# Kernel optimization log

Hardware: AMD Instinct MI355X
Metric: run time of the kernel (lower is better)

The kernel has to match this reference:

```python
import jax, jax.numpy as jnp
from jax import lax
import numpy as np

N_ASSETS = 256
BATCH = 512
MAX_WEIGHT = 0.05
N_ITERS = 300       # FISTA iterations (fixed, jit-friendly)
BISECT_ITERS = 60   # bisection iterations for the simplex-box projection
POWER_ITERS = 30    # power iterations for Lipschitz constant


def _project_capped_simplex(v, c):
    """Project rows of v onto {w : sum(w)=1, -c <= w <= c}.

    Finds tau s.t. sum(clip(v - tau, -c, c)) = 1 by bisection (non-diff),
    then recomputes tau exactly from the active-set mask so the projection
    is correctly differentiable (piecewise-linear Jacobian).
    """
    vs = lax.stop_gradient(v)
    lo = jnp.min(vs, axis=-1) - c   # sum = +n*c > 1 here
    hi = jnp.max(vs, axis=-1) + c   # sum = -n*c < 1 here

    def bis(carry, _):
        lo, hi = carry
        mid = 0.5 * (lo + hi)
        s = jnp.sum(jnp.clip(vs - mid[:, None], -c, c), axis=-1)
        lo = jnp.where(s > 1.0, mid, lo)
        hi = jnp.where(s > 1.0, hi, mid)
        return (lo, hi), None

    (lo, hi), _ = lax.scan(bis, (lo, hi), None, length=BISECT_ITERS)
    tau0 = 0.5 * (lo + hi)
    z = vs - tau0[:, None]
    interior = (jnp.abs(z) < c).astype(v.dtype)          # unclipped coords
    k_hi = jnp.sum((z >= c).astype(v.dtype), axis=-1)    # clipped at +c
    k_lo = jnp.sum((z <= -c).astype(v.dtype), axis=-1)   # clipped at -c
    denom = jnp.maximum(jnp.sum(interior, axis=-1), 1.0)
    # exact tau given the (stop-gradient) active set -> correct Jacobian in v
    tau = (jnp.sum(interior * v, axis=-1) + c * (k_hi - k_lo) - 1.0) / denom
    return jnp.clip(v - tau[:, None], -c, c)


def _min_var_weights(covmat_sqrt, c):
    """argmin_w ||A w||^2  s.t. sum(w)=1, -c<=w<=c  (batched FISTA)."""
    B, n, _ = covmat_sqrt.shape
    # Q = A^T A (the objective only depends on A through Q)
    Q = jnp.einsum('bij,bik->bjk', covmat_sqrt, covmat_sqrt)

    # power iteration for lambda_max(Q) -> step size 1/L, L = 2*lambda_max
    u = jnp.ones((B, n), covmat_sqrt.dtype) / jnp.sqrt(jnp.asarray(n, covmat_sqrt.dtype))

    def pit(u, _):
        u = jnp.einsum('bij,bj->bi', Q, u)
        u = u / (jnp.linalg.norm(u, axis=-1, keepdims=True) + 1e-12)
        return u, None

    u, _ = lax.scan(pit, u, None, length=POWER_ITERS)
    lmax = jnp.einsum('bi,bij,bj->b', u, Q, u)
    step = lax.stop_gradient(1.0 / (2.0 * lmax + 1e-12))[:, None]

    w0 = _project_capped_simplex(jnp.full((B, n), 1.0 / n, covmat_sqrt.dtype), c)

    @jax.checkpoint
    def fista(carry, _):
        w, y, t = carry
        g = 2.0 * jnp.einsum('bij,bj->bi', Q, y)
        w_new = _project_capped_simplex(y - step * g, c)
        t_new = 0.5 * (1.0 + jnp.sqrt(1.0 + 4.0 * t * t))
        y_new = w_new + ((t - 1.0) / t_new) * (w_new - w)
        return (w_new, y_new, t_new), None

    t0 = jnp.asarray(1.0, covmat_sqrt.dtype)
    (w, _, _), _ = lax.scan(fista, (w0, w0, t0), None, length=N_ITERS)
    return w


def setup_inputs() -> dict:
    key = jax.random.key(0)
    covmat_sqrt = jax.random.normal(
        key, (BATCH, N_ASSETS, N_ASSETS), dtype=jnp.float32
    ) / np.sqrt(N_ASSETS).astype(np.float32)
    return {"covmat_sqrt": covmat_sqrt}


def reference(covmat_sqrt):
    return _min_var_weights(covmat_sqrt, MAX_WEIGHT)
```

## Files before the change

kernel.cpp:

```cpp
#include <hip/hip_runtime.h>
#include <math.h>


#define NA    256
#define CAPW  0.05f

typedef float v2f __attribute__((ext_vector_type(2)));

template<int CTRL, int RM>
__device__ __forceinline__ float dpp0(float x) {
    return __int_as_float(__builtin_amdgcn_update_dpp(
        0, __float_as_int(x), CTRL, RM, 0xf, true));
}
template<int CTRL, int RM>
__device__ __forceinline__ float dppI(float x, float ident) {
    return __int_as_float(__builtin_amdgcn_update_dpp(
        __float_as_int(ident), __float_as_int(x), CTRL, RM, 0xf, false));
}
__device__ __forceinline__ float bcast63(float x) {
    return __int_as_float(__builtin_amdgcn_readlane(__float_as_int(x), 63));
}
__device__ __forceinline__ float wsum(float x) {
    x += dpp0<0x111, 0xf>(x);
    x += dpp0<0x112, 0xf>(x);
    x += dpp0<0x114, 0xf>(x);
    x += dpp0<0x118, 0xf>(x);
    x += dpp0<0x142, 0xa>(x);
    x += dpp0<0x143, 0xc>(x);
    return bcast63(x);
}
__device__ __forceinline__ float wmin(float x) {
    const float I = 1e30f;
    x = fminf(x, dppI<0x111, 0xf>(x, I));
    x = fminf(x, dppI<0x112, 0xf>(x, I));
    x = fminf(x, dppI<0x114, 0xf>(x, I));
    x = fminf(x, dppI<0x118, 0xf>(x, I));
    x = fminf(x, dppI<0x142, 0xa>(x, I));
    x = fminf(x, dppI<0x143, 0xc>(x, I));
    return bcast63(x);
}
__device__ __forceinline__ float wmax(float x) {
    const float I = -1e30f;
    x = fmaxf(x, dppI<0x111, 0xf>(x, I));
    x = fmaxf(x, dppI<0x112, 0xf>(x, I));
    x = fmaxf(x, dppI<0x114, 0xf>(x, I));
    x = fmaxf(x, dppI<0x118, 0xf>(x, I));
    x = fmaxf(x, dppI<0x142, 0xa>(x, I));
    x = fmaxf(x, dppI<0x143, 0xc>(x, I));
    return bcast63(x);
}

__global__ void __launch_bounds__(512, 2)
markowitz_fista(const float* __restrict__ A, float* __restrict__ out)
{
    __shared__ float A_lds[32 * 256];
    __shared__ float y_lds[256];
    __shared__ float p_lds[8 * 256];
    __shared__ int   done_flag;

    const int tid = threadIdx.x;
    const int b   = blockIdx.x;
    const int r4  = tid & 63;
    const int e   = tid >> 6;
    const int R0  = r4 * 4;
    const int C0  = e * 32;

    const float* __restrict__ Ab = A + (size_t)b * NA * NA;

    v2f q2[4][16];
    #pragma unroll
    for (int a = 0; a < 4; ++a)
        #pragma unroll
        for (int k = 0; k < 16; ++k) q2[a][k] = (v2f){0.0f, 0.0f};

    for (int it = 0; it < 8; ++it) {
        __syncthreads();
        const float4* src = (const float4*)(Ab + it * 32 * 256);
        float4* dst = (float4*)A_lds;
        #pragma unroll
        for (int qd = 0; qd < 4; ++qd) dst[qd * 512 + tid] = src[qd * 512 + tid];
        __syncthreads();
        for (int ii = 0; ii < 32; ++ii) {
            const float* row = A_lds + ii * 256;
            float4 rv = *(const float4*)(row + R0);
            v2f r0 = {rv.x, rv.x}, r1 = {rv.y, rv.y}, r2 = {rv.z, rv.z}, r3 = {rv.w, rv.w};
            #pragma unroll
            for (int cc = 0; cc < 8; ++cc) {
                float4 cv = *(const float4*)(row + C0 + 4 * cc);
                v2f clo = {cv.x, cv.y}, chi = {cv.z, cv.w};
                q2[0][2*cc  ] = __builtin_elementwise_fma(r0, clo, q2[0][2*cc  ]);
                q2[0][2*cc+1] = __builtin_elementwise_fma(r0, chi, q2[0][2*cc+1]);
                q2[1][2*cc  ] = __builtin_elementwise_fma(r1, clo, q2[1][2*cc  ]);
                q2[1][2*cc+1] = __builtin_elementwise_fma(r1, chi, q2[1][2*cc+1]);
                q2[2][2*cc  ] = __builtin_elementwise_fma(r2, clo, q2[2][2*cc  ]);
                q2[2][2*cc+1] = __builtin_elementwise_fma(r2, chi, q2[2][2*cc+1]);
                q2[3][2*cc  ] = __builtin_elementwise_fma(r3, clo, q2[3][2*cc  ]);
                q2[3][2*cc+1] = __builtin_elementwise_fma(r3, chi, q2[3][2*cc+1]);
            }
        }
    }

    auto partials = [&](bool chk) -> bool {
        __syncthreads();
        int fl = chk ? done_flag : 0;
        v2f aL0 = {0,0}, aL1 = {0,0}, aL2 = {0,0}, aL3 = {0,0};
        v2f aH0 = {0,0}, aH1 = {0,0}, aH2 = {0,0}, aH3 = {0,0};
        const float* yv = y_lds + C0;
        #pragma unroll
        for (int cc = 0; cc < 8; ++cc) {
            float4 y4 = *(const float4*)(yv + 4 * cc);
            v2f ylo = {y4.x, y4.y}, yhi = {y4.z, y4.w};
            aL0 = __builtin_elementwise_fma(q2[0][2*cc  ], ylo, aL0);
            aH0 = __builtin_elementwise_fma(q2[0][2*cc+1], yhi, aH0);
            aL1 = __builtin_elementwise_fma(q2[1][2*cc  ], ylo, aL1);
            aH1 = __builtin_elementwise_fma(q2[1][2*cc+1], yhi, aH1);
            aL2 = __builtin_elementwise_fma(q2[2][2*cc  ], ylo, aL2);
            aH2 = __builtin_elementwise_fma(q2[2][2*cc+1], yhi, aH2);
            aL3 = __builtin_elementwise_fma(q2[3][2*cc  ], ylo, aL3);
            aH3 = __builtin_elementwise_fma(q2[3][2*cc+1], yhi, aH3);
        }
        if (fl) return true;
        v2f s0 = aL0 + aH0, s1 = aL1 + aH1, s2 = aL2 + aH2, s3 = aL3 + aH3;
        *(float4*)(p_lds + e * 256 + R0) =
            make_float4(s0.x + s0.y, s1.x + s1.y, s2.x + s2.y, s3.x + s3.y);
        __syncthreads();
        return false;
    };
    auto reduceg = [&]() -> float4 {
        float4 r = *(const float4*)(p_lds + 4 * tid);
        #pragma unroll
        for (int ee = 1; ee < 8; ++ee) {
            float4 pv = *(const float4*)(p_lds + ee * 256 + 4 * tid);
            r.x += pv.x; r.y += pv.y; r.z += pv.z; r.w += pv.w;
        }
        return r;
    };

    if (tid < 64) {
        *(float4*)(y_lds + 4 * tid) = make_float4(0.0625f, 0.0625f, 0.0625f, 0.0625f);
    }
    float u0 = 0.f, u1 = 0.f, u2 = 0.f, u3 = 0.f;
    for (int p = 0; p < 30; ++p) {
        partials(false);
        if (tid < 64) {
            float4 g4 = reduceg();
            float ss = wsum(g4.x*g4.x + g4.y*g4.y + g4.z*g4.z + g4.w*g4.w);
            float inv = 1.0f / (sqrtf(ss) + 1e-12f);
            u0 = g4.x * inv; u1 = g4.y * inv; u2 = g4.z * inv; u3 = g4.w * inv;
            *(float4*)(y_lds + 4 * tid) = make_float4(u0, u1, u2, u3);
        }
    }
    partials(false);

    float step2 = 0.f, t = 1.0f, tau_ws = 0.0f, rm = 0.0f;
    float wa = 0.f, wb = 0.f, wc = 0.f, wd = 0.f;
    float ya = 0.f, yb = 0.f, yc = 0.f, yd = 0.f;
    if (tid < 64) {
        float4 g4 = reduceg();
        float lm = wsum(u0*g4.x + u1*g4.y + u2*g4.z + u3*g4.w);
        float step = 1.0f / (2.0f * lm + 1e-12f);
        step2 = 2.0f * step;
        wa = wb = wc = wd = 1.0f / 256.0f;
        ya = yb = yc = yd = 1.0f / 256.0f;
        *(float4*)(y_lds + 4 * tid) = make_float4(ya, yb, yc, yd);
    }
    if (tid == 0) done_flag = 0;

    for (int itn = 0; itn < 300; ++itn) {
        if (partials(true)) break;
        if (tid < 64) {
            float4 g4 = reduceg();
            float v0 = ya - step2 * g4.x;
            float v1 = yb - step2 * g4.y;
            float v2 = yc - step2 * g4.z;
            float v3 = yd - step2 * g4.w;

            float lo = wmin(fminf(fminf(v0, v1), fminf(v2, v3))) - CAPW;
            float hi = wmax(fmaxf(fmaxf(v0, v1), fmaxf(v2, v3))) + CAPW;
            float tau = fminf(fmaxf(tau_ws, lo), hi);

            float s = 0.f, cnt = 1.f, sm1 = 0.f;
            bool have = false;
            for (int ni = 0; ni < 10; ++ni) {
                float z0 = v0 - tau, z1 = v1 - tau, z2 = v2 - tau, z3 = v3 - tau;
                float c0 = fminf(fmaxf(z0, -CAPW), CAPW);
                float c1 = fminf(fmaxf(z1, -CAPW), CAPW);
                float c2 = fminf(fmaxf(z2, -CAPW), CAPW);
                float c3 = fminf(fmaxf(z3, -CAPW), CAPW);
                s   = wsum(c0 + c1 + c2 + c3);
                cnt = wsum((fabsf(z0) < CAPW ? 1.f : 0.f) +
                           (fabsf(z1) < CAPW ? 1.f : 0.f) +
                           (fabsf(z2) < CAPW ? 1.f : 0.f) +
                           (fabsf(z3) < CAPW ? 1.f : 0.f));
                sm1 = s - 1.0f;
                if (fabsf(sm1) <= 1e-5f) { have = true; break; }
                if (sm1 > 0.0f) lo = tau; else hi = tau;
                float tn2 = tau + sm1 / fmaxf(cnt, 1.0f);
                if (!(tn2 > lo && tn2 < hi)) tn2 = 0.5f * (lo + hi);
                tau = tn2;
            }
            if (!have) {
                float z0 = v0 - tau, z1 = v1 - tau, z2 = v2 - tau, z3 = v3 - tau;
                float c0 = fminf(fmaxf(z0, -CAPW), CAPW);
                float c1 = fminf(fmaxf(z1, -CAPW), CAPW);
                float c2 = fminf(fmaxf(z2, -CAPW), CAPW);
                float c3 = fminf(fmaxf(z3, -CAPW), CAPW);
                s   = wsum(c0 + c1 + c2 + c3);
                cnt = wsum((fabsf(z0) < CAPW ? 1.f : 0.f) +
                           (fabsf(z1) < CAPW ? 1.f : 0.f) +
                           (fabsf(z2) < CAPW ? 1.f : 0.f) +
                           (fabsf(z3) < CAPW ? 1.f : 0.f));
                sm1 = s - 1.0f;
            }
            float tauf = tau + sm1 / fmaxf(cnt, 1.0f);
            tau_ws = tauf;
            float w0n = fminf(fmaxf(v0 - tauf, -CAPW), CAPW);
            float w1n = fminf(fmaxf(v1 - tauf, -CAPW), CAPW);
            float w2n = fminf(fmaxf(v2 - tauf, -CAPW), CAPW);
            float w3n = fminf(fmaxf(v3 - tauf, -CAPW), CAPW);

            float tn = 0.5f * (1.0f + sqrtf(1.0f + 4.0f * t * t));
            float beta = (t - 1.0f) / tn;
            float y0n = w0n + beta * (w0n - wa);
            float y1n = w1n + beta * (w1n - wb);
            float y2n = w2n + beta * (w2n - wc);
            float y3n = w3n + beta * (w3n - wd);

            float dm = fmaxf(fmaxf(fabsf(w0n - wa), fabsf(w1n - wb)),
                             fmaxf(fabsf(w2n - wc), fabsf(w3n - wd)));
            rm = fmaxf(rm, dm);
            if ((itn & 7) == 7) {
                float rmax = wmax(rm);
                if (rmax < 1e-10f && tid == 0) done_flag = 1;
                rm = 0.0f;
            }

            wa = w0n; wb = w1n; wc = w2n; wd = w3n;
            ya = y0n; yb = y1n; yc = y2n; yd = y3n;
            t = tn;
            *(float4*)(y_lds + 4 * tid) = make_float4(ya, yb, yc, yd);
        }
    }

    if (tid < 64) {
        *(float4*)(out + b * 256 + 4 * tid) = make_float4(wa, wb, wc, wd);
    }
}

extern "C" void kernel_launch(void* const* d_in, const int* in_sizes, int n_in,
                              void* d_out, int out_size, void* d_ws, size_t ws_size,
                              hipStream_t stream) {
    (void)in_sizes; (void)n_in; (void)d_ws; (void)ws_size; (void)out_size;
    const float* A = (const float*)d_in[0];
    float* out = (float*)d_out;
    hipLaunchKernelGGL(markowitz_fista, dim3(512), dim3(512), 0, stream, A, out);
}
```

Measured before the change: 1.058 ms.

## Run projection redundantly in all waves and double-buffer partials to cut barriers

Every wave now redundantly performs the gradient reduction and capped-simplex projection, rather than only wave 0. Each wave publishes only the y slice that it itself consumes, so no cross-wave y handoff is needed. Partial sums are double-buffered, which lets each iteration use a single barrier instead of two, and the done flag becomes a per-wave early break. This removes idle waves waiting on wave 0 and one barrier per iteration, at the cost of duplicated scalar work and more LDS reads in the reduction.

```diff
diff --git a/kernel.cpp b/kernel.cpp
--- a/kernel.cpp
+++ b/kernel.cpp
@@ -54,16 +54,15 @@
 markowitz_fista(const float* __restrict__ A, float* __restrict__ out)
 {
     __shared__ float A_lds[32 * 256];
-    __shared__ float y_lds[256];
-    __shared__ float p_lds[8 * 256];
-    __shared__ int   done_flag;
-
-    const int tid = threadIdx.x;
-    const int b   = blockIdx.x;
-    const int r4  = tid & 63;
-    const int e   = tid >> 6;
-    const int R0  = r4 * 4;
-    const int C0  = e * 32;
+    __shared__ float p_lds[2][8 * 256];
+    __shared__ float y_sl[8 * 32];
+
+    const int tid  = threadIdx.x;
+    const int b    = blockIdx.x;
+    const int lane = tid & 63;
+    const int e    = tid >> 6;
+    const int R0   = lane * 4;
+    const int C0   = e * 32;
 
     const float* __restrict__ Ab = A + (size_t)b * NA * NA;
 
@@ -100,12 +99,15 @@
         }
     }
 
-    auto partials = [&](bool chk) -> bool {
-        __syncthreads();
-        int fl = chk ? done_flag : 0;
+    auto publish_y = [&](float y0v, float y1v, float y2v, float y3v) {
+        if ((lane >> 3) == e)
+            *(float4*)(y_sl + C0 + ((lane & 7) << 2)) = make_float4(y0v, y1v, y2v, y3v);
+    };
+
+    auto partials = [&](int buf) {
         v2f aL0 = {0,0}, aL1 = {0,0}, aL2 = {0,0}, aL3 = {0,0};
         v2f aH0 = {0,0}, aH1 = {0,0}, aH2 = {0,0}, aH3 = {0,0};
-        const float* yv = y_lds + C0;
+        const float* yv = y_sl + C0;
         #pragma unroll
         for (int cc = 0; cc < 8; ++cc) {
             float4 y4 = *(const float4*)(yv + 4 * cc);
@@ -119,131 +121,123 @@
             aL3 = __builtin_elementwise_fma(q2[3][2*cc  ], ylo, aL3);
             aH3 = __builtin_elementwise_fma(q2[3][2*cc+1], yhi, aH3);
         }
-        if (fl) return true;
         v2f s0 = aL0 + aH0, s1 = aL1 + aH1, s2 = aL2 + aH2, s3 = aL3 + aH3;
-        *(float4*)(p_lds + e * 256 + R0) =
+        *(float4*)(&p_lds[buf][e * 256 + R0]) =
             make_float4(s0.x + s0.y, s1.x + s1.y, s2.x + s2.y, s3.x + s3.y);
         __syncthreads();
-        return false;
     };
-    auto reduceg = [&]() -> float4 {
-        float4 r = *(const float4*)(p_lds + 4 * tid);
+    auto reduceg = [&](int buf) -> float4 {
+        float4 r = *(const float4*)(&p_lds[buf][R0]);
         #pragma unroll
         for (int ee = 1; ee < 8; ++ee) {
-            float4 pv = *(const float4*)(p_lds + ee * 256 + 4 * tid);
+            float4 pv = *(const float4*)(&p_lds[buf][ee * 256 + R0]);
             r.x += pv.x; r.y += pv.y; r.z += pv.z; r.w += pv.w;
         }
         return r;
     };
 
-    if (tid < 64) {
-        *(float4*)(y_lds + 4 * tid) = make_float4(0.0625f, 0.0625f, 0.0625f, 0.0625f);
-    }
-    float u0 = 0.f, u1 = 0.f, u2 = 0.f, u3 = 0.f;
+    float u0 = 0.0625f, u1 = 0.0625f, u2 = 0.0625f, u3 = 0.0625f;
+    publish_y(u0, u1, u2, u3);
+    int pb = 0;
     for (int p = 0; p < 30; ++p) {
-        partials(false);
-        if (tid < 64) {
-            float4 g4 = reduceg();
-            float ss = wsum(g4.x*g4.x + g4.y*g4.y + g4.z*g4.z + g4.w*g4.w);
-            float inv = 1.0f / (sqrtf(ss) + 1e-12f);
-            u0 = g4.x * inv; u1 = g4.y * inv; u2 = g4.z * inv; u3 = g4.w * inv;
-            *(float4*)(y_lds + 4 * tid) = make_float4(u0, u1, u2, u3);
-        }
-    }
-    partials(false);
-
-    float step2 = 0.f, t = 1.0f, tau_ws = 0.0f, rm = 0.0f;
-    float wa = 0.f, wb = 0.f, wc = 0.f, wd = 0.f;
-    float ya = 0.f, yb = 0.f, yc = 0.f, yd = 0.f;
-    if (tid < 64) {
-        float4 g4 = reduceg();
+        partials(pb);
+        float4 g4 = reduceg(pb); pb ^= 1;
+        float ss = wsum(g4.x*g4.x + g4.y*g4.y + g4.z*g4.z + g4.w*g4.w);
+        float inv = 1.0f / (sqrtf(ss) + 1e-12f);
+        u0 = g4.x * inv; u1 = g4.y * inv; u2 = g4.z * inv; u3 = g4.w * inv;
+        publish_y(u0, u1, u2, u3);
+    }
+    partials(pb);
+    {
+        float4 g4 = reduceg(pb); pb ^= 1;
         float lm = wsum(u0*g4.x + u1*g4.y + u2*g4.z + u3*g4.w);
         float step = 1.0f / (2.0f * lm + 1e-12f);
-        step2 = 2.0f * step;
-        wa = wb = wc = wd = 1.0f / 256.0f;
-        ya = yb = yc = yd = 1.0f / 256.0f;
-        *(float4*)(y_lds + 4 * tid) = make_float4(ya, yb, yc, yd);
-    }
-    if (tid == 0) done_flag = 0;
+        u0 = 2.0f * step;
+    }
+    const float step2 = u0;
+
+    float t = 1.0f, tau_ws = 0.0f, rm = 0.0f;
+    float wa = 1.0f/256.0f, wb = wa, wc = wa, wd = wa;
+    float ya = wa, yb = wa, yc = wa, yd = wa;
+    publish_y(ya, yb, yc, yd);
 
     for (int itn = 0; itn < 300; ++itn) {
-        if (partials(true)) break;
-        if (tid < 64) {
-            float4 g4 = reduceg();
-            float v0 = ya - step2 * g4.x;
-            float v1 = yb - step2 * g4.y;
-            float v2 = yc - step2 * g4.z;
-            float v3 = yd - step2 * g4.w;
-
-            float lo = wmin(fminf(fminf(v0, v1), fminf(v2, v3))) - CAPW;
-            float hi = wmax(fmaxf(fmaxf(v0, v1), fmaxf(v2, v3))) + CAPW;
-            float tau = fminf(fmaxf(tau_ws, lo), hi);
-
-            float s = 0.f, cnt = 1.f, sm1 = 0.f;
-            bool have = false;
-            for (int ni = 0; ni < 10; ++ni) {
-                float z0 = v0 - tau, z1 = v1 - tau, z2 = v2 - tau, z3 = v3 - tau;
-                float c0 = fminf(fmaxf(z0, -CAPW), CAPW);
-                float c1 = fminf(fmaxf(z1, -CAPW), CAPW);
-                float c2 = fminf(fmaxf(z2, -CAPW), CAPW);
-                float c3 = fminf(fmaxf(z3, -CAPW), CAPW);
-                s   = wsum(c0 + c1 + c2 + c3);
-                cnt = wsum((fabsf(z0) < CAPW ? 1.f : 0.f) +
-                           (fabsf(z1) < CAPW ? 1.f : 0.f) +
-                           (fabsf(z2) < CAPW ? 1.f : 0.f) +
-                           (fabsf(z3) < CAPW ? 1.f : 0.f));
-                sm1 = s - 1.0f;
-                if (fabsf(sm1) <= 1e-5f) { have = true; break; }
-                if (sm1 > 0.0f) lo = tau; else hi = tau;
-                float tn2 = tau + sm1 / fmaxf(cnt, 1.0f);
-                if (!(tn2 > lo && tn2 < hi)) tn2 = 0.5f * (lo + hi);
-                tau = tn2;
-            }
-            if (!have) {
-                float z0 = v0 - tau, z1 = v1 - tau, z2 = v2 - tau, z3 = v3 - tau;
-                float c0 = fminf(fmaxf(z0, -CAPW), CAPW);
-                float c1 = fminf(fmaxf(z1, -CAPW), CAPW);
-                float c2 = fminf(fmaxf(z2, -CAPW), CAPW);
-                float c3 = fminf(fmaxf(z3, -CAPW), CAPW);
-                s   = wsum(c0 + c1 + c2 + c3);
-                cnt = wsum((fabsf(z0) < CAPW ? 1.f : 0.f) +
-                           (fabsf(z1) < CAPW ? 1.f : 0.f) +
-                           (fabsf(z2) < CAPW ? 1.f : 0.f) +
-                           (fabsf(z3) < CAPW ? 1.f : 0.f));
-                sm1 = s - 1.0f;
-            }
-            float tauf = tau + sm1 / fmaxf(cnt, 1.0f);
-            tau_ws = tauf;
-            float w0n = fminf(fmaxf(v0 - tauf, -CAPW), CAPW);
-            float w1n = fminf(fmaxf(v1 - tauf, -CAPW), CAPW);
-            float w2n = fminf(fmaxf(v2 - tauf, -CAPW), CAPW);
-            float w3n = fminf(fmaxf(v3 - tauf, -CAPW), CAPW);
-
-            float tn = 0.5f * (1.0f + sqrtf(1.0f + 4.0f * t * t));
-            float beta = (t - 1.0f) / tn;
-            float y0n = w0n + beta * (w0n - wa);
-            float y1n = w1n + beta * (w1n - wb);
-            float y2n = w2n + beta * (w2n - wc);
-            float y3n = w3n + beta * (w3n - wd);
-
-            float dm = fmaxf(fmaxf(fabsf(w0n - wa), fabsf(w1n - wb)),
-                             fmaxf(fabsf(w2n - wc), fabsf(w3n - wd)));
-            rm = fmaxf(rm, dm);
-            if ((itn & 7) == 7) {
-                float rmax = wmax(rm);
-                if (rmax < 1e-10f && tid == 0) done_flag = 1;
-                rm = 0.0f;
-            }
-
-            wa = w0n; wb = w1n; wc = w2n; wd = w3n;
-            ya = y0n; yb = y1n; yc = y2n; yd = y3n;
-            t = tn;
-            *(float4*)(y_lds + 4 * tid) = make_float4(ya, yb, yc, yd);
+        partials(pb);
+        float4 g4 = reduceg(pb); pb ^= 1;
+        float v0 = ya - step2 * g4.x;
+        float v1 = yb - step2 * g4.y;
+        float v2 = yc - step2 * g4.z;
+        float v3 = yd - step2 * g4.w;
+
+        float lo = wmin(fminf(fminf(v0, v1), fminf(v2, v3))) - CAPW;
+        float hi = wmax(fmaxf(fmaxf(v0, v1), fmaxf(v2, v3))) + CAPW;
+        float tau = fminf(fmaxf(tau_ws, lo), hi);
+
+        float s = 0.f, cnt = 1.f, sm1 = 0.f;
+        bool have = false;
+        for (int ni = 0; ni < 10; ++ni) {
+            float z0 = v0 - tau, z1 = v1 - tau, z2 = v2 - tau, z3 = v3 - tau;
+            float c0 = fminf(fmaxf(z0, -CAPW), CAPW);
+            float c1 = fminf(fmaxf(z1, -CAPW), CAPW);
+            float c2 = fminf(fmaxf(z2, -CAPW), CAPW);
+            float c3 = fminf(fmaxf(z3, -CAPW), CAPW);
+            s   = wsum(c0 + c1 + c2 + c3);
+            cnt = wsum((fabsf(z0) < CAPW ? 1.f : 0.f) +
+                       (fabsf(z1) < CAPW ? 1.f : 0.f) +
+                       (fabsf(z2) < CAPW ? 1.f : 0.f) +
+                       (fabsf(z3) < CAPW ? 1.f : 0.f));
+            sm1 = s - 1.0f;
+            if (fabsf(sm1) <= 1e-5f) { have = true; break; }
+            if (sm1 > 0.0f) lo = tau; else hi = tau;
+            float tn2 = tau + sm1 / fmaxf(cnt, 1.0f);
+            if (!(tn2 > lo && tn2 < hi)) tn2 = 0.5f * (lo + hi);
+            tau = tn2;
+        }
+        if (!have) {
+            float z0 = v0 - tau, z1 = v1 - tau, z2 = v2 - tau, z3 = v3 - tau;
+            float c0 = fminf(fmaxf(z0, -CAPW), CAPW);
+            float c1 = fminf(fmaxf(z1, -CAPW), CAPW);
+            float c2 = fminf(fmaxf(z2, -CAPW), CAPW);
+            float c3 = fminf(fmaxf(z3, -CAPW), CAPW);
+            s   = wsum(c0 + c1 + c2 + c3);
+            cnt = wsum((fabsf(z0) < CAPW ? 1.f : 0.f) +
+                       (fabsf(z1) < CAPW ? 1.f : 0.f) +
+                       (fabsf(z2) < CAPW ? 1.f : 0.f) +
+                       (fabsf(z3) < CAPW ? 1.f : 0.f));
+            sm1 = s - 1.0f;
+        }
+        float tauf = tau + sm1 / fmaxf(cnt, 1.0f);
+        tau_ws = tauf;
+        float w0n = fminf(fmaxf(v0 - tauf, -CAPW), CAPW);
+        float w1n = fminf(fmaxf(v1 - tauf, -CAPW), CAPW);
+        float w2n = fminf(fmaxf(v2 - tauf, -CAPW), CAPW);
+        float w3n = fminf(fmaxf(v3 - tauf, -CAPW), CAPW);
+
+        float tn = 0.5f * (1.0f + sqrtf(1.0f + 4.0f * t * t));
+        float beta = (t - 1.0f) / tn;
+        float y0n = w0n + beta * (w0n - wa);
+        float y1n = w1n + beta * (w1n - wb);
+        float y2n = w2n + beta * (w2n - wc);
+        float y3n = w3n + beta * (w3n - wd);
+
+        float dm = fmaxf(fmaxf(fabsf(w0n - wa), fabsf(w1n - wb)),
+                         fmaxf(fabsf(w2n - wc), fabsf(w3n - wd)));
+        rm = fmaxf(rm, dm);
+
+        wa = w0n; wb = w1n; wc = w2n; wd = w3n;
+        ya = y0n; yb = y1n; yc = y2n; yd = y3n;
+        t = tn;
+        publish_y(ya, yb, yc, yd);
+
+        if ((itn & 7) == 7) {
+            float rmax = wmax(rm);
+            rm = 0.0f;
+            if (rmax < 1e-10f) break;
         }
     }
 
     if (tid < 64) {
-        *(float4*)(out + b * 256 + 4 * tid) = make_float4(wa, wb, wc, wd);
+        *(float4*)(out + b * 256 + R0) = make_float4(wa, wb, wc, wd);
     }
 }
 
```

New measurement: 1.245 ms. +17.7%, slower.
